# Performance work log

Hardware: AMD Instinct MI355X
Metric: run time of the kernel (lower is better)

Reference implementation:

```python
import jax, jax.numpy as jnp
import numpy as np

N = 100000   # nodes
E = 1600000  # edges
IN = 128     # in_node_channels
H = 128      # hidden_channels
EPS = 1e-5   # BatchNorm eps


def _gcn_conv(x, W, b, src, dst, n):
    # x' = W x, then symmetric-normalized aggregation with self-loops (PyG GCNConv)
    xw = x @ W                                             # [N, H]
    loop = jnp.arange(n, dtype=src.dtype)
    src_f = jnp.concatenate([src, loop])                   # [E+N]
    dst_f = jnp.concatenate([dst, loop])
    deg = jax.ops.segment_sum(jnp.ones(src_f.shape, xw.dtype), dst_f, num_segments=n)
    dis = jax.lax.rsqrt(jnp.maximum(deg, 1.0))             # deg >= 1 due to self-loops
    norm = dis[src_f] * dis[dst_f]                         # [E+N]
    msg = xw[src_f] * norm[:, None]                        # gather + scale
    out = jax.ops.segment_sum(msg, dst_f, num_segments=n)  # scatter-add
    return out + b


def _bn(x, gamma, beta):
    # training-mode BatchNorm1d over the node dimension
    m = jnp.mean(x, axis=0)
    v = jnp.mean(jnp.square(x - m), axis=0)
    return gamma * (x - m) * jax.lax.rsqrt(v + EPS) + beta


def setup_inputs() -> dict:
    key = jax.random.key(0)
    ks = jax.random.split(key, 8)
    glorot = lambda k, shape, fan: jax.random.normal(k, shape, jnp.float32) / np.sqrt(fan).astype(np.float32)
    x = jax.random.normal(ks[0], (N, IN), jnp.float32)
    edge_index = jax.random.randint(ks[1], (2, E), 0, N, dtype=jnp.int32)
    return {
        "x": x,
        "edge_index": edge_index,
        "W1": glorot(ks[2], (IN, H), IN), "b1": jnp.zeros((H,), jnp.float32),
        "g1": jnp.ones((H,), jnp.float32), "be1": jnp.zeros((H,), jnp.float32),
        "W2": glorot(ks[3], (H, H), H), "b2": jnp.zeros((H,), jnp.float32),
        "g2": jnp.ones((H,), jnp.float32), "be2": jnp.zeros((H,), jnp.float32),
        "Wm1": glorot(ks[4], (H, 64), H), "bm1": jnp.zeros((64,), jnp.float32),
        "Wm2": glorot(ks[5], (64, 1), 64), "bm2": jnp.zeros((1,), jnp.float32),
    }


def reference(x, edge_index, W1, b1, g1, be1, W2, b2, g2, be2, Wm1, bm1, Wm2, bm2):
    src, dst = edge_index[0], edge_index[1]
    h = jax.nn.relu(_bn(_gcn_conv(x, W1, b1, src, dst, N), g1, be1))
    h = jax.nn.relu(_bn(_gcn_conv(h, W2, b2, src, dst, N), g2, be2))
    # MLP head (dropout is identity in eval / deterministic reference)
    h = jax.nn.relu(h @ Wm1 + bm1)
    out = h @ Wm2 + bm2                                     # [N, 1]
    return jnp.squeeze(out, axis=-1)                        # [N]
```

## Files before the change

### kernel.cpp

```cpp
#include <hip/hip_runtime.h>
#include <hip/hip_fp16.h>

#define HC 128
#define EPS_BN 1e-5f
#define NSTRIPE 8
#define AGG_BLOCKS 3072
#define BSHIFT 9
#define BNODES (1 << BSHIFT)
#define CHUNK 8192
#define SRC_BITS 18

typedef _Float16 f16;
typedef f16  f16x8 __attribute__((ext_vector_type(8)));
typedef float f32x4 __attribute__((ext_vector_type(4)));

__global__ __launch_bounds__(256) void bucket_count(const int* __restrict__ dst,
                                                    int* __restrict__ bcnt, int E) {
    __shared__ int c[256];
    const int tid = threadIdx.x;
    const int e0 = blockIdx.x * CHUNK;
    c[tid] = 0;
    __syncthreads();
    for (int i = tid; i < CHUNK; i += 256) {
        int e = e0 + i;
        if (e < E) atomicAdd(&c[dst[e] >> BSHIFT], 1);
    }
    __syncthreads();
    if (c[tid] > 0) atomicAdd(&bcnt[tid], c[tid]);
}

__global__ __launch_bounds__(256) void bscan(const int* __restrict__ bcnt,
                                             int* __restrict__ bbase, int* __restrict__ gcur,
                                             int* __restrict__ rowptr, int nb, int n, int E) {
    __shared__ int s[256];
    const int tid = threadIdx.x;
    s[tid] = (tid < nb) ? bcnt[tid] : 0;
    __syncthreads();
    for (int off = 1; off < 256; off <<= 1) {
        int t = (tid >= off) ? s[tid - off] : 0;
        __syncthreads();
        s[tid] += t;
        __syncthreads();
    }
    int excl = tid ? s[tid - 1] : 0;
    if (tid < nb) { bbase[tid] = excl; gcur[tid] = excl; }
    if (tid == 0) { bbase[nb] = E; rowptr[n] = E; }
}

__global__ __launch_bounds__(256) void edge_bin(const int* __restrict__ src,
                                                const int* __restrict__ dst,
                                                int* __restrict__ gcur,
                                                unsigned int* __restrict__ packed, int E) {
    __shared__ int cnt[256];
    __shared__ int cur[256];
    const int tid = threadIdx.x;
    const int e0 = blockIdx.x * CHUNK;
    cnt[tid] = 0;
    __syncthreads();
    for (int i = tid; i < CHUNK; i += 256) {
        int e = e0 + i;
        if (e < E) atomicAdd(&cnt[dst[e] >> BSHIFT], 1);
    }
    __syncthreads();
    cur[tid] = (cnt[tid] > 0) ? atomicAdd(&gcur[tid], cnt[tid]) : 0;
    __syncthreads();
    for (int i = tid; i < CHUNK; i += 256) {
        int e = e0 + i;
        if (e < E) {
            int s = src[e], d = dst[e];
            int pos = atomicAdd(&cur[d >> BSHIFT], 1);
            packed[pos] = ((unsigned)(d & (BNODES - 1)) << SRC_BITS) | (unsigned)s;
        }
    }
}

__global__ __launch_bounds__(256) void edge_sort(const unsigned int* __restrict__ packed,
                                                 const int* __restrict__ bbase,
                                                 int* __restrict__ rowptr,
                                                 float* __restrict__ dis,
                                                 int* __restrict__ srcs, int n) {
    __shared__ int cnt[BNODES];
    __shared__ int cur[BNODES];
    __shared__ int scn[256];
    const int b = blockIdx.x;
    const int node0 = b << BSHIFT;
    const int tid = threadIdx.x;
    const int base = bbase[b];
    const int end  = bbase[b + 1];

    cnt[tid] = 0; cnt[tid + 256] = 0;
    __syncthreads();
    for (int e = base + tid; e < end; e += 256)
        atomicAdd(&cnt[packed[e] >> SRC_BITS], 1);
    __syncthreads();
    int p0 = cnt[2 * tid], p1 = cnt[2 * tid + 1];
    scn[tid] = p0 + p1;
    __syncthreads();
    for (int off = 1; off < 256; off <<= 1) {
        int t = (tid >= off) ? scn[tid - off] : 0;
        __syncthreads();
        scn[tid] += t;
        __syncthreads();
    }
    int eb = tid ? scn[tid - 1] : 0;
    {
        int nodeA = node0 + 2 * tid;
        int nodeB = nodeA + 1;
        if (nodeA < n) { rowptr[nodeA] = base + eb;      dis[nodeA] = rsqrtf((float)p0 + 1.f); }
        if (nodeB < n) { rowptr[nodeB] = base + eb + p0; dis[nodeB] = rsqrtf((float)p1 + 1.f); }
    }
    cur[2 * tid] = eb;
    cur[2 * tid + 1] = eb + p0;
    __syncthreads();
    for (int e = base + tid; e < end; e += 256) {
        unsigned p = packed[e];
        int pos = atomicAdd(&cur[p >> SRC_BITS], 1);
        srcs[base + pos] = (int)(p & ((1u << SRC_BITS) - 1));
    }
}

__global__ void wprep_all(const float* __restrict__ W1, const float* __restrict__ W2,
                          const float* __restrict__ Wm1,
                          f16* __restrict__ Wt1, f16* __restrict__ Wt2,
                          f16* __restrict__ Wm1t, f16* __restrict__ padrow) {
    int idx = blockIdx.x * 256 + threadIdx.x;
    if (idx < 16384) {
        int k = idx >> 7, c = idx & 127;
        Wt1[(size_t)c * HC + k] = (f16)W1[idx];
    } else if (idx < 32768) {
        int i = idx - 16384;
        int k = i >> 7, c = i & 127;
        Wt2[(size_t)c * HC + k] = (f16)W2[i];
    } else if (idx < 40960) {
        int i = idx - 32768;
        int c = i >> 7, k = i & 127;
        Wm1t[(size_t)c * HC + k] = (f16)Wm1[(size_t)k * 64 + c];
    } else if (idx < 41088) {
        padrow[idx - 40960] = (f16)0.f;
    }
}

template<int SRC_F16, int TRANS>
__global__ __launch_bounds__(256) void gemm_mfma(const void* __restrict__ Xv,
                                                 const f16* __restrict__ Wt,
                                                 const float* __restrict__ stats,
                                                 const float* __restrict__ gamma,
                                                 const float* __restrict__ beta,
                                                 const float* __restrict__ dis,
                                                 f16* __restrict__ Y, int n) {
    __shared__ f16 Ah[64][136];
    __shared__ f16 Bh[128][136];
    __shared__ float sc[HC], sh[HC];
    const int tid  = threadIdx.x;
    const int row0 = blockIdx.x * 64;

    if constexpr (TRANS) {
        if (tid < 128) {
            float s = 0.f, q = 0.f;
#pragma unroll
            for (int t = 0; t < NSTRIPE; ++t) {
                s += stats[t * 256 + tid];
                q += stats[t * 256 + 128 + tid];
            }
            float m = s / (float)n;
            float v = q / (float)n - m * m;
            float scv = gamma[tid] * rsqrtf(fmaxf(v, 0.f) + EPS_BN);
            sc[tid] = scv;
            sh[tid] = beta[tid] - m * scv;
        }
    }

#pragma unroll
    for (int i = 0; i < 8; ++i) {
        int idx = i * 256 + tid;
        int r = idx >> 4, g = idx & 15;
        *(f16x8*)&Bh[r][g * 8] = *(const f16x8*)(Wt + (size_t)r * HC + g * 8);
    }
    __syncthreads();

#pragma unroll
    for (int i = 0; i < 4; ++i) {
        int idx = i * 256 + tid;
        int r = idx >> 4, g = idx & 15;
        int grow = row0 + r;
        f16x8 h = {};
        if (grow < n) {
            if constexpr (SRC_F16) {
                f16x8 v = *(const f16x8*)((const f16*)Xv + (size_t)grow * HC + g * 8);
                if constexpr (TRANS) {
#pragma unroll
                    for (int j = 0; j < 8; ++j) {
                        float f = (float)v[j];
                        f = fmaxf(fmaf(f, sc[g * 8 + j], sh[g * 8 + j]), 0.f);
                        h[j] = (f16)f;
                    }
                } else h = v;
            } else {
                const float* X = (const float*)Xv;
                float4 a = *(const float4*)(X + (size_t)grow * HC + g * 8);
                float4 c = *(const float4*)(X + (size_t)grow * HC + g * 8 + 4);
                h[0] = (f16)a.x; h[1] = (f16)a.y; h[2] = (f16)a.z; h[3] = (f16)a.w;
                h[4] = (f16)c.x; h[5] = (f16)c.y; h[6] = (f16)c.z; h[7] = (f16)c.w;
            }
        }
        *(f16x8*)&Ah[r][g * 8] = h;
    }
    __syncthreads();

    const int wv   = tid >> 6;
    const int lane = tid & 63;
    const int m    = lane & 15;
    const int kq   = (lane >> 4) * 8;

    f32x4 acc[8] = {};
#pragma unroll
    for (int kc = 0; kc < HC; kc += 32) {
        f16x8 a = *(const f16x8*)&Ah[wv * 16 + m][kc + kq];
#pragma unroll
        for (int t = 0; t < 8; ++t) {
            f16x8 b = *(const f16x8*)&Bh[t * 16 + m][kc + kq];
            acc[t] = __builtin_amdgcn_mfma_f32_16x16x32_f16(a, b, acc[t], 0, 0, 0);
        }
    }

    const int rbase = row0 + wv * 16 + (lane >> 4) * 4;
#pragma unroll
    for (int r = 0; r < 4; ++r) {
        int grow = rbase + r;
        if (grow < n) {
            float dv = dis[grow];
#pragma unroll
            for (int t = 0; t < 8; ++t)
                Y[(size_t)grow * HC + t * 16 + m] = (f16)(acc[t][r] * dv);
        }
    }
}

__global__ __launch_bounds__(256) void gcn_agg_f16(const f16* __restrict__ xws,
                                                   const int* __restrict__ srcs,
                                                   const int* __restrict__ rowptr,
                                                   const float* __restrict__ dis,
                                                   const float* __restrict__ bias,
                                                   f16* __restrict__ out,
                                                   float* __restrict__ stats,
                                                   int n, int nwaves) {
    __shared__ float lds_s[4][128], lds_q[4][128];
    const int wv   = threadIdx.x >> 6;
    const int lane = threadIdx.x & 63;
    const int g    = lane >> 4;
    const int cg   = lane & 15;

    float b8[8];
#pragma unroll
    for (int j = 0; j < 8; ++j) b8[j] = bias[cg * 8 + j];

    float s8[8] = {}, q8[8] = {};

    for (int node = blockIdx.x * 4 + wv; node < n; node += nwaves) {
        const int e0 = rowptr[node];
        const int e1 = rowptr[node + 1];
        float acc[8] = {};
        for (int e = e0; e < e1; e += 16) {
            int i0 = e + g;
            int s0 = (i0      < e1) ? srcs[i0]      : n;
            int s1 = (i0 + 4  < e1) ? srcs[i0 + 4]  : n;
            int s2 = (i0 + 8  < e1) ? srcs[i0 + 8]  : n;
            int s3 = (i0 + 12 < e1) ? srcs[i0 + 12] : n;
            f16x8 v0 = *(const f16x8*)(xws + (size_t)s0 * HC + cg * 8);
            f16x8 v1 = *(const f16x8*)(xws + (size_t)s1 * HC + cg * 8);
            f16x8 v2 = *(const f16x8*)(xws + (size_t)s2 * HC + cg * 8);
            f16x8 v3 = *(const f16x8*)(xws + (size_t)s3 * HC + cg * 8);
#pragma unroll
            for (int j = 0; j < 8; ++j)
                acc[j] += ((float)v0[j] + (float)v1[j]) + ((float)v2[j] + (float)v3[j]);
        }
#pragma unroll
        for (int j = 0; j < 8; ++j) acc[j] += __shfl_xor(acc[j], 16);
#pragma unroll
        for (int j = 0; j < 8; ++j) acc[j] += __shfl_xor(acc[j], 32);

        if (g == 0) {
            float dv = dis[node];
            f16x8 self = *(const f16x8*)(xws + (size_t)node * HC + cg * 8);
            f16x8 o;
#pragma unroll
            for (int j = 0; j < 8; ++j) {
                float r = fmaf(acc[j] + (float)self[j], dv, b8[j]);
                o[j] = (f16)r;
                s8[j] += r;
                q8[j] += r * r;
            }
            *(f16x8*)(out + (size_t)node * HC + cg * 8) = o;
        }
    }

    if (g == 0) {
#pragma unroll
        for (int j = 0; j < 8; ++j) {
            lds_s[wv][cg * 8 + j] = s8[j];
            lds_q[wv][cg * 8 + j] = q8[j];
        }
    }
    __syncthreads();
    float* stripe = stats + (size_t)(blockIdx.x & (NSTRIPE - 1)) * 256;
    if (threadIdx.x < 128) {
        float s = lds_s[0][threadIdx.x] + lds_s[1][threadIdx.x] +
                  lds_s[2][threadIdx.x] + lds_s[3][threadIdx.x];
        float q = lds_q[0][threadIdx.x] + lds_q[1][threadIdx.x] +
                  lds_q[2][threadIdx.x] + lds_q[3][threadIdx.x];
        atomicAdd(&stripe[threadIdx.x], s);
        atomicAdd(&stripe[128 + threadIdx.x], q);
    }
}

__global__ __launch_bounds__(256) void mlp_mfma(const f16* __restrict__ h,
                                                const float* __restrict__ stats,
                                                const float* __restrict__ gamma,
                                                const float* __restrict__ beta,
                                                const f16* __restrict__ Wm1t,
                                                const float* __restrict__ bm1,
                                                const float* __restrict__ Wm2,
                                                const float* __restrict__ bm2,
                                                float* __restrict__ out, int n) {
    __shared__ f16 Hs[64][136];
    __shared__ f16 Ws[64][136];
    __shared__ float sc[HC], sh[HC], bmv[64], w2v[64];
    const int tid  = threadIdx.x;
    const int row0 = blockIdx.x * 64;

    if (tid < 128) {
        float s = 0.f, q = 0.f;
#pragma unroll
        for (int t = 0; t < NSTRIPE; ++t) {
            s += stats[t * 256 + tid];
            q += stats[t * 256 + 128 + tid];
        }
        float m = s / (float)n;
        float v = q / (float)n - m * m;
        float scv = gamma[tid] * rsqrtf(fmaxf(v, 0.f) + EPS_BN);
        sc[tid] = scv;
        sh[tid] = beta[tid] - m * scv;
    }
    if (tid < 64) { bmv[tid] = bm1[tid]; w2v[tid] = Wm2[tid]; }

#pragma unroll
    for (int i = 0; i < 4; ++i) {
        int idx = i * 256 + tid;
        int r = idx >> 4, g = idx & 15;
        *(f16x8*)&Ws[r][g * 8] = *(const f16x8*)(Wm1t + (size_t)r * HC + g * 8);
    }
    __syncthreads();

#pragma unroll
    for (int i = 0; i < 4; ++i) {
        int idx = i * 256 + tid;
        int r = idx >> 4, g = idx & 15;
        int grow = row0 + r;
        f16x8 hv = {};
        if (grow < n) {
            f16x8 v = *(const f16x8*)(h + (size_t)grow * HC + g * 8);
#pragma unroll
            for (int j = 0; j < 8; ++j) {
                float f = (float)v[j];
                f = fmaxf(fmaf(f, sc[g * 8 + j], sh[g * 8 + j]), 0.f);
                hv[j] = (f16)f;
            }
        }
        *(f16x8*)&Hs[r][g * 8] = hv;
    }
    __syncthreads();

    const int wv   = tid >> 6;
    const int lane = tid & 63;
    const int m    = lane & 15;
    const int kq   = (lane >> 4) * 8;

    f32x4 acc[4] = {};
#pragma unroll
    for (int kc = 0; kc < HC; kc += 32) {
        f16x8 a = *(const f16x8*)&Hs[wv * 16 + m][kc + kq];
#pragma unroll
        for (int t = 0; t < 4; ++t) {
            f16x8 b = *(const f16x8*)&Ws[t * 16 + m][kc + kq];
            acc[t] = __builtin_amdgcn_mfma_f32_16x16x32_f16(a, b, acc[t], 0, 0, 0);
        }
    }

    float part[4];
#pragma unroll
    for (int reg = 0; reg < 4; ++reg) {
        float s = 0.f;
#pragma unroll
        for (int t = 0; t < 4; ++t) {
            int col = t * 16 + m;
            s += fmaxf(acc[t][reg] + bmv[col], 0.f) * w2v[col];
        }
        part[reg] = s;
    }
#pragma unroll
    for (int off = 1; off < 16; off <<= 1) {
#pragma unroll
        for (int reg = 0; reg < 4; ++reg)
            part[reg] += __shfl_xor(part[reg], off);
    }
    if (m == 0) {
        int rbase = row0 + wv * 16 + (lane >> 4) * 4;
        float bb = bm2[0];
#pragma unroll
        for (int reg = 0; reg < 4; ++reg) {
            int row = rbase + reg;
            if (row < n) out[row] = part[reg] + bb;
        }
    }
}

extern "C" void kernel_launch(void* const* d_in, const int* in_sizes, int n_in,
                              void* d_out, int out_size, void* d_ws, size_t ws_size,
                              hipStream_t stream) {
    const float* x   = (const float*)d_in[0];
    const int*   ei  = (const int*)  d_in[1];
    const float* W1  = (const float*)d_in[2];
    const float* b1  = (const float*)d_in[3];
    const float* g1  = (const float*)d_in[4];
    const float* be1 = (const float*)d_in[5];
    const float* W2  = (const float*)d_in[6];
    const float* b2  = (const float*)d_in[7];
    const float* g2  = (const float*)d_in[8];
    const float* be2 = (const float*)d_in[9];
    const float* Wm1 = (const float*)d_in[10];
    const float* bm1 = (const float*)d_in[11];
    const float* Wm2 = (const float*)d_in[12];
    const float* bm2 = (const float*)d_in[13];
    float* out = (float*)d_out;

    const int n = in_sizes[0] / HC;
    const int E = in_sizes[1] / 2;
    const int* srcp = ei;
    const int* dstp = ei + E;
    const int nb = (n + BNODES - 1) >> BSHIFT;

    char* ws = (char*)d_ws;
    size_t off = 0;
    auto alloc = [&](size_t bytes) { void* p = ws + off; off = (off + bytes + 511) & ~511ULL; return p; };
    float*  dis    = (float*) alloc((size_t)n * 4);
    int*    rowptr = (int*)   alloc((size_t)(n + 1) * 4);
    int*    bcnt   = (int*)   alloc(1024);
    int*    bbase  = (int*)   alloc(1024 + 4);
    int*    gcur   = (int*)   alloc(1024);
    unsigned int* packed = (unsigned int*)alloc((size_t)E * 4);
    int*    srcs   = (int*)   alloc((size_t)E * 4);
    f16*    xws    = (f16*)   alloc((size_t)(n + 1) * HC * 2);
    f16*    bufBh  = (f16*)   alloc((size_t)n * HC * 2);
    f16*    Wt1    = (f16*)   alloc((size_t)HC * HC * 2);
    f16*    Wt2    = (f16*)   alloc((size_t)HC * HC * 2);
    f16*    Wm1t   = (f16*)   alloc((size_t)64 * HC * 2);
    float*  stats1 = (float*) alloc(NSTRIPE * 256 * 4);
    float*  stats2 = (float*) alloc(NSTRIPE * 256 * 4);

    const int gemmBlocks = (n + 63) / 64;
    const int binBlocks  = (E + CHUNK - 1) / CHUNK;
    const int aggWaves   = AGG_BLOCKS * 4;

    hipMemsetAsync(bcnt, 0, 1024, stream);
    hipMemsetAsync(stats1, 0, NSTRIPE * 256 * 4, stream);
    hipMemsetAsync(stats2, 0, NSTRIPE * 256 * 4, stream);

    bucket_count<<<binBlocks, 256, 0, stream>>>(dstp, bcnt, E);
    bscan<<<1, 256, 0, stream>>>(bcnt, bbase, gcur, rowptr, nb, n, E);
    edge_bin<<<binBlocks, 256, 0, stream>>>(srcp, dstp, gcur, packed, E);
    edge_sort<<<nb, 256, 0, stream>>>(packed, bbase, rowptr, dis, srcs, n);

    wprep_all<<<(41088 + 255) / 256, 256, 0, stream>>>(W1, W2, Wm1, Wt1, Wt2, Wm1t,
                                                       xws + (size_t)n * HC);

    gemm_mfma<0, 0><<<gemmBlocks, 256, 0, stream>>>(x, Wt1, nullptr, nullptr, nullptr,
                                                    dis, xws, n);
    gcn_agg_f16<<<AGG_BLOCKS, 256, 0, stream>>>(xws, srcs, rowptr, dis, b1,
                                                bufBh, stats1, n, aggWaves);

    gemm_mfma<1, 1><<<gemmBlocks, 256, 0, stream>>>(bufBh, Wt2, stats1, g1, be1,
                                                    dis, xws, n);
    gcn_agg_f16<<<AGG_BLOCKS, 256, 0, stream>>>(xws, srcs, rowptr, dis, b2,
                                                bufBh, stats2, n, aggWaves);

    mlp_mfma<<<gemmBlocks, 256, 0, stream>>>(bufBh, stats2, g2, be2, Wm1t, bm1, Wm2, bm2,
                                             out, n);
}
```

Measured before the change: 363.1 us.

## Use 1024-thread blocks for edge binning, halve aggregation unroll, merge memsets

The bucket count, edge bin and edge sort kernels now launch with 1024 threads per block, and edge_sort does a per-node 512-wide scan instead of the paired 256-wide scan. This gives the CSR build more parallelism per block, since only 196 blocks run in the sort. The aggregation inner loop now gathers 2 rows per lane per iteration instead of 4, trading memory-level parallelism for lower register pressure. Three memsets are merged into one over a single contiguous zeroed region, saving launch overhead.

```diff
diff --git a/kernel.cpp b/kernel.cpp
--- a/kernel.cpp
+++ b/kernel.cpp
@@ -14,19 +14,19 @@
 typedef f16  f16x8 __attribute__((ext_vector_type(8)));
 typedef float f32x4 __attribute__((ext_vector_type(4)));
 
-__global__ __launch_bounds__(256) void bucket_count(const int* __restrict__ dst,
-                                                    int* __restrict__ bcnt, int E) {
+__global__ __launch_bounds__(1024) void bucket_count(const int* __restrict__ dst,
+                                                     int* __restrict__ bcnt, int E) {
     __shared__ int c[256];
     const int tid = threadIdx.x;
     const int e0 = blockIdx.x * CHUNK;
-    c[tid] = 0;
-    __syncthreads();
-    for (int i = tid; i < CHUNK; i += 256) {
+    if (tid < 256) c[tid] = 0;
+    __syncthreads();
+    for (int i = tid; i < CHUNK; i += 1024) {
         int e = e0 + i;
         if (e < E) atomicAdd(&c[dst[e] >> BSHIFT], 1);
     }
     __syncthreads();
-    if (c[tid] > 0) atomicAdd(&bcnt[tid], c[tid]);
+    if (tid < 256 && c[tid] > 0) atomicAdd(&bcnt[tid], c[tid]);
 }
 
 __global__ __launch_bounds__(256) void bscan(const int* __restrict__ bcnt,
@@ -47,24 +47,24 @@
     if (tid == 0) { bbase[nb] = E; rowptr[n] = E; }
 }
 
-__global__ __launch_bounds__(256) void edge_bin(const int* __restrict__ src,
-                                                const int* __restrict__ dst,
-                                                int* __restrict__ gcur,
-                                                unsigned int* __restrict__ packed, int E) {
+__global__ __launch_bounds__(1024) void edge_bin(const int* __restrict__ src,
+                                                 const int* __restrict__ dst,
+                                                 int* __restrict__ gcur,
+                                                 unsigned int* __restrict__ packed, int E) {
     __shared__ int cnt[256];
     __shared__ int cur[256];
     const int tid = threadIdx.x;
     const int e0 = blockIdx.x * CHUNK;
-    cnt[tid] = 0;
-    __syncthreads();
-    for (int i = tid; i < CHUNK; i += 256) {
+    if (tid < 256) cnt[tid] = 0;
+    __syncthreads();
+    for (int i = tid; i < CHUNK; i += 1024) {
         int e = e0 + i;
         if (e < E) atomicAdd(&cnt[dst[e] >> BSHIFT], 1);
     }
     __syncthreads();
-    cur[tid] = (cnt[tid] > 0) ? atomicAdd(&gcur[tid], cnt[tid]) : 0;
-    __syncthreads();
-    for (int i = tid; i < CHUNK; i += 256) {
+    if (tid < 256) cur[tid] = (cnt[tid] > 0) ? atomicAdd(&gcur[tid], cnt[tid]) : 0;
+    __syncthreads();
+    for (int i = tid; i < CHUNK; i += 1024) {
         int e = e0 + i;
         if (e < E) {
             int s = src[e], d = dst[e];
@@ -74,45 +74,45 @@
     }
 }
 
-__global__ __launch_bounds__(256) void edge_sort(const unsigned int* __restrict__ packed,
-                                                 const int* __restrict__ bbase,
-                                                 int* __restrict__ rowptr,
-                                                 float* __restrict__ dis,
-                                                 int* __restrict__ srcs, int n) {
+__global__ __launch_bounds__(1024) void edge_sort(const unsigned int* __restrict__ packed,
+                                                  const int* __restrict__ bbase,
+                                                  int* __restrict__ rowptr,
+                                                  float* __restrict__ dis,
+                                                  int* __restrict__ srcs, int n) {
     __shared__ int cnt[BNODES];
     __shared__ int cur[BNODES];
-    __shared__ int scn[256];
+    __shared__ int scn[BNODES];
     const int b = blockIdx.x;
     const int node0 = b << BSHIFT;
     const int tid = threadIdx.x;
     const int base = bbase[b];
     const int end  = bbase[b + 1];
 
-    cnt[tid] = 0; cnt[tid + 256] = 0;
-    __syncthreads();
-    for (int e = base + tid; e < end; e += 256)
+    if (tid < BNODES) cnt[tid] = 0;
+    __syncthreads();
+    for (int e = base + tid; e < end; e += 1024)
         atomicAdd(&cnt[packed[e] >> SRC_BITS], 1);
     __syncthreads();
-    int p0 = cnt[2 * tid], p1 = cnt[2 * tid + 1];
-    scn[tid] = p0 + p1;
-    __syncthreads();
-    for (int off = 1; off < 256; off <<= 1) {
-        int t = (tid >= off) ? scn[tid - off] : 0;
+    if (tid < BNODES) scn[tid] = cnt[tid];
+    __syncthreads();
+    for (int off = 1; off < BNODES; off <<= 1) {
+        int t = 0;
+        if (tid < BNODES && tid >= off) t = scn[tid - off];
         __syncthreads();
-        scn[tid] += t;
+        if (tid < BNODES) scn[tid] += t;
         __syncthreads();
     }
-    int eb = tid ? scn[tid - 1] : 0;
-    {
-        int nodeA = node0 + 2 * tid;
-        int nodeB = nodeA + 1;
-        if (nodeA < n) { rowptr[nodeA] = base + eb;      dis[nodeA] = rsqrtf((float)p0 + 1.f); }
-        if (nodeB < n) { rowptr[nodeB] = base + eb + p0; dis[nodeB] = rsqrtf((float)p1 + 1.f); }
-    }
-    cur[2 * tid] = eb;
-    cur[2 * tid + 1] = eb + p0;
-    __syncthreads();
-    for (int e = base + tid; e < end; e += 256) {
+    if (tid < BNODES) {
+        int excl = scn[tid] - cnt[tid];
+        int node = node0 + tid;
+        if (node < n) {
+            rowptr[node] = base + excl;
+            dis[node] = rsqrtf((float)cnt[tid] + 1.f);
+        }
+        cur[tid] = excl;
+    }
+    __syncthreads();
+    for (int e = base + tid; e < end; e += 1024) {
         unsigned p = packed[e];
         int pos = atomicAdd(&cur[p >> SRC_BITS], 1);
         srcs[base + pos] = (int)(p & ((1u << SRC_BITS) - 1));
@@ -260,19 +260,17 @@
         const int e0 = rowptr[node];
         const int e1 = rowptr[node + 1];
         float acc[8] = {};
-        for (int e = e0; e < e1; e += 16) {
-            int i0 = e + g;
-            int s0 = (i0      < e1) ? srcs[i0]      : n;
-            int s1 = (i0 + 4  < e1) ? srcs[i0 + 4]  : n;
-            int s2 = (i0 + 8  < e1) ? srcs[i0 + 8]  : n;
-            int s3 = (i0 + 12 < e1) ? srcs[i0 + 12] : n;
+        for (int e = e0; e < e1; e += 8) {
+            int i0 = e + g, i1 = e + g + 4;
+            int s0 = (i0 < e1) ? srcs[i0] : n;
+            int s1 = (i1 < e1) ? srcs[i1] : n;
             f16x8 v0 = *(const f16x8*)(xws + (size_t)s0 * HC + cg * 8);
             f16x8 v1 = *(const f16x8*)(xws + (size_t)s1 * HC + cg * 8);
-            f16x8 v2 = *(const f16x8*)(xws + (size_t)s2 * HC + cg * 8);
-            f16x8 v3 = *(const f16x8*)(xws + (size_t)s3 * HC + cg * 8);
-#pragma unroll
-            for (int j = 0; j < 8; ++j)
-                acc[j] += ((float)v0[j] + (float)v1[j]) + ((float)v2[j] + (float)v3[j]);
+#pragma unroll
+            for (int j = 0; j < 8; ++j) {
+                acc[j] += (float)v0[j];
+                acc[j] += (float)v1[j];
+            }
         }
 #pragma unroll
         for (int j = 0; j < 8; ++j) acc[j] += __shfl_xor(acc[j], 16);
@@ -444,7 +442,10 @@
     auto alloc = [&](size_t bytes) { void* p = ws + off; off = (off + bytes + 511) & ~511ULL; return p; };
     float*  dis    = (float*) alloc((size_t)n * 4);
     int*    rowptr = (int*)   alloc((size_t)(n + 1) * 4);
-    int*    bcnt   = (int*)   alloc(1024);
+    int*    zreg   = (int*)   alloc((256 + 2 * NSTRIPE * 256) * 4);
+    int*    bcnt   = zreg;
+    float*  stats1 = (float*)(zreg + 256);
+    float*  stats2 = stats1 + NSTRIPE * 256;
     int*    bbase  = (int*)   alloc(1024 + 4);
     int*    gcur   = (int*)   alloc(1024);
     unsigned int* packed = (unsigned int*)alloc((size_t)E * 4);
@@ -454,21 +455,17 @@
     f16*    Wt1    = (f16*)   alloc((size_t)HC * HC * 2);
     f16*    Wt2    = (f16*)   alloc((size_t)HC * HC * 2);
     f16*    Wm1t   = (f16*)   alloc((size_t)64 * HC * 2);
-    float*  stats1 = (float*) alloc(NSTRIPE * 256 * 4);
-    float*  stats2 = (float*) alloc(NSTRIPE * 256 * 4);
 
     const int gemmBlocks = (n + 63) / 64;
     const int binBlocks  = (E + CHUNK - 1) / CHUNK;
     const int aggWaves   = AGG_BLOCKS * 4;
 
-    hipMemsetAsync(bcnt, 0, 1024, stream);
-    hipMemsetAsync(stats1, 0, NSTRIPE * 256 * 4, stream);
-    hipMemsetAsync(stats2, 0, NSTRIPE * 256 * 4, stream);
-
-    bucket_count<<<binBlocks, 256, 0, stream>>>(dstp, bcnt, E);
+    hipMemsetAsync(zreg, 0, (256 + 2 * NSTRIPE * 256) * 4, stream);
+
+    bucket_count<<<binBlocks, 1024, 0, stream>>>(dstp, bcnt, E);
     bscan<<<1, 256, 0, stream>>>(bcnt, bbase, gcur, rowptr, nb, n, E);
-    edge_bin<<<binBlocks, 256, 0, stream>>>(srcp, dstp, gcur, packed, E);
-    edge_sort<<<nb, 256, 0, stream>>>(packed, bbase, rowptr, dis, srcs, n);
+    edge_bin<<<binBlocks, 1024, 0, stream>>>(srcp, dstp, gcur, packed, E);
+    edge_sort<<<nb, 1024, 0, stream>>>(packed, bbase, rowptr, dis, srcs, n);
 
     wprep_all<<<(41088 + 255) / 256, 256, 0, stream>>>(W1, W2, Wm1, Wt1, Wt2, Wm1t,
                                                        xws + (size_t)n * HC);
```

New measurement: 329.6 us. -9.2%, faster.
